# Performance work log

Measured on AMD Instinct MI355X. Metric: run time of the kernel, lower is better.

Reference implementation:

```python
import jax, jax.numpy as jnp
import numpy as np

D_MODEL = 1024
N_HEADS = 16
D_HEAD = D_MODEL // N_HEADS
D_FF = 4 * D_MODEL
EPS = 1e-5


def _layernorm(x, g, b):
    mu = jnp.mean(x, axis=-1, keepdims=True)
    var = jnp.var(x, axis=-1, keepdims=True)
    return (x - mu) * jax.lax.rsqrt(var + EPS) * g + b


def setup_inputs() -> dict:
    key = jax.random.key(0)
    ks = jax.random.split(key, 16)
    s_attn = 1.0 / np.sqrt(D_MODEL)
    s_ff1 = 1.0 / np.sqrt(D_MODEL)
    s_ff2 = 1.0 / np.sqrt(D_FF)
    inp = {
        'x': jax.random.normal(ks[0], (2, 2048, D_MODEL), dtype=jnp.float32),
        'Wq': jax.random.uniform(ks[1], (D_MODEL, D_MODEL), jnp.float32, -s_attn, s_attn),
        'bq': jax.random.uniform(ks[2], (D_MODEL,), jnp.float32, -s_attn, s_attn),
        'Wk': jax.random.uniform(ks[3], (D_MODEL, D_MODEL), jnp.float32, -s_attn, s_attn),
        'bk': jax.random.uniform(ks[4], (D_MODEL,), jnp.float32, -s_attn, s_attn),
        'Wv': jax.random.uniform(ks[5], (D_MODEL, D_MODEL), jnp.float32, -s_attn, s_attn),
        'bv': jax.random.uniform(ks[6], (D_MODEL,), jnp.float32, -s_attn, s_attn),
        'Wo': jax.random.uniform(ks[7], (D_MODEL, D_MODEL), jnp.float32, -s_attn, s_attn),
        'bo': jax.random.uniform(ks[8], (D_MODEL,), jnp.float32, -s_attn, s_attn),
        'W1': jax.random.uniform(ks[9], (D_MODEL, D_FF), jnp.float32, -s_ff1, s_ff1),
        'b1': jax.random.uniform(ks[10], (D_FF,), jnp.float32, -s_ff1, s_ff1),
        'W2': jax.random.uniform(ks[11], (D_FF, D_MODEL), jnp.float32, -s_ff2, s_ff2),
        'b2': jax.random.uniform(ks[12], (D_MODEL,), jnp.float32, -s_ff2, s_ff2),
        'ln1_g': jnp.ones((D_MODEL,), jnp.float32),
        'ln1_b': jnp.zeros((D_MODEL,), jnp.float32),
        'ln2_g': jnp.ones((D_MODEL,), jnp.float32),
        'ln2_b': jnp.zeros((D_MODEL,), jnp.float32),
    }
    return inp


def reference(x, Wq, bq, Wk, bk, Wv, bv, Wo, bo, W1, b1, W2, b2, ln1_g, ln1_b, ln2_g, ln2_b):
    B, T, D = x.shape
    scale = D_HEAD ** -0.5

    # pre-norm MHSA + residual
    h = _layernorm(x, ln1_g, ln1_b)
    def split(z):  # [B,T,D] -> [B,H,T,d_h]
        return z.reshape(B, T, N_HEADS, D_HEAD).transpose(0, 2, 1, 3)
    Q = split(h @ Wq + bq)
    K = split(h @ Wk + bk)
    V = split(h @ Wv + bv)
    scores = jnp.einsum('bhqd,bhkd->bhqk', Q, K) * scale  # [B,H,T,T]
    attn = jax.nn.softmax(scores, axis=-1)
    out = jnp.einsum('bhqk,bhkd->bhqd', attn, V)
    out = out.transpose(0, 2, 1, 3).reshape(B, T, D)
    x = x + (out @ Wo + bo)

    # pre-norm FFN + residual
    h = _layernorm(x, ln2_g, ln2_b)
    ff = jax.nn.gelu(h @ W1 + b1, approximate=False) @ W2 + b2
    return x + ff
```

## Files before the change

### kernel.cpp

```cpp
#include <hip/hip_runtime.h>
#include <math.h>

#define SEQ   2048
#define DM    1024
#define LDQKV 3072
#define MTOK  4096

typedef float  f32x4   __attribute__((ext_vector_type(4)));
typedef __bf16 bf16x8  __attribute__((ext_vector_type(8)));
typedef short  short8  __attribute__((ext_vector_type(8)));
typedef short  short4v __attribute__((ext_vector_type(4)));

__device__ __forceinline__ short f2bf(float f) {
  union { float f; unsigned u; } v; v.f = f;
  unsigned r = v.u + 0x7fffu + ((v.u >> 16) & 1u);
  return (short)(r >> 16);
}

__device__ __forceinline__ void gl_lds16(const void* g, void* l) {
  __builtin_amdgcn_global_load_lds(
      (const __attribute__((address_space(1))) void*)g,
      (__attribute__((address_space(3))) void*)l, 16, 0, 0);
}

__device__ __forceinline__ f32x4 mfma_bf16(bf16x8 a, bf16x8 b, f32x4 c) {
  return __builtin_amdgcn_mfma_f32_16x16x32_bf16(a, b, c, 0, 0, 0);
}

__global__ __launch_bounds__(256) void transpose_cast_k(
    const float* __restrict__ W, short* __restrict__ Wt, int K, int N)
{
  __shared__ float tile[32][33];
  const int n0 = blockIdx.x * 32, k0 = blockIdx.y * 32;
  const int tx = threadIdx.x & 31, ty = threadIdx.x >> 5;
#pragma unroll
  for (int i = 0; i < 4; i++)
    tile[ty + i * 8][tx] = W[(size_t)(k0 + ty + i * 8) * N + n0 + tx];
  __syncthreads();
#pragma unroll
  for (int i = 0; i < 4; i++)
    Wt[(size_t)(n0 + ty + i * 8) * K + k0 + tx] = f2bf(tile[tx][ty + i * 8]);
}

__global__ __launch_bounds__(256) void ln_k(
    const float* __restrict__ x, const float* __restrict__ g,
    const float* __restrict__ b, short* __restrict__ out)
{
  const int row = blockIdx.x;
  const int tid = threadIdx.x;
  const float4 v = ((const float4*)(x + (size_t)row * DM))[tid];
  float s  = v.x + v.y + v.z + v.w;
  float ss = v.x * v.x + v.y * v.y + v.z * v.z + v.w * v.w;
#pragma unroll
  for (int m = 32; m >= 1; m >>= 1) { s += __shfl_xor(s, m); ss += __shfl_xor(ss, m); }
  __shared__ float red[8];
  const int wid = tid >> 6;
  if ((tid & 63) == 0) { red[wid] = s; red[4 + wid] = ss; }
  __syncthreads();
  s  = red[0] + red[1] + red[2] + red[3];
  ss = red[4] + red[5] + red[6] + red[7];
  const float mu  = s * (1.f / DM);
  const float var = ss * (1.f / DM) - mu * mu;
  const float rs  = rsqrtf(var + 1e-5f);
  const float4 gv = ((const float4*)g)[tid];
  const float4 bv = ((const float4*)b)[tid];
  short4v o;
  o[0] = f2bf((v.x - mu) * rs * gv.x + bv.x);
  o[1] = f2bf((v.y - mu) * rs * gv.y + bv.y);
  o[2] = f2bf((v.z - mu) * rs * gv.z + bv.z);
  o[3] = f2bf((v.w - mu) * rs * gv.w + bv.w);
  *(short4v*)(out + (size_t)row * DM + tid * 4) = o;
}

__global__ __launch_bounds__(256) void concat_bias_k(
    const float* __restrict__ bq, const float* __restrict__ bk,
    const float* __restrict__ bv, float* __restrict__ o)
{
  int i = blockIdx.x * 256 + threadIdx.x;
  if (i < 3072) {
    float v = (i < 1024) ? bq[i] : (i < 2048 ? bk[i - 1024] : bv[i - 2048]);
    o[i] = v;
  }
}

__global__ __launch_bounds__(256) void vtrans_k(
    const short* __restrict__ V, short* __restrict__ Vt)
{
  const int b = blockIdx.z, h = blockIdx.y, t0 = blockIdx.x * 64;
  __shared__ short tile[64][72];
  const int tid = threadIdx.x;
  const int r = tid >> 2, c = (tid & 3) * 16;
  const short* src = V + (size_t)(b * SEQ + t0 + r) * LDQKV + h * 64 + c;
  *(short8*)&tile[r][c]     = *(const short8*)src;
  *(short8*)&tile[r][c + 8] = *(const short8*)(src + 8);
  __syncthreads();
  const int d = tid >> 2;
  short8 o0, o1;
#pragma unroll
  for (int k = 0; k < 8; k++) o0[k] = tile[c + k][d];
#pragma unroll
  for (int k = 0; k < 8; k++) o1[k] = tile[c + 8 + k][d];
  short* dst = Vt + (((size_t)(b * 16 + h) * 64) + d) * 2048 + t0 + c;
  *(short8*)dst       = o0;
  *(short8*)(dst + 8) = o1;
}

template <bool GELU_, bool RESID, bool OUTBF16>
__global__ __launch_bounds__(256) void gemm_bt(
    const short* __restrict__ A, const short* __restrict__ Bt,
    const float* __restrict__ bias, const float* __restrict__ resid,
    void* __restrict__ Cout, int M, int N, int K)
{
  __shared__ __align__(16) short Abuf[2][128 * 32];
  __shared__ __align__(16) short Bbuf[2][128 * 32];
  const int tid = threadIdx.x, lane = tid & 63, wid = tid >> 6;
  const int wr = wid >> 1, wc = wid & 1;
  const int bm = blockIdx.x * 128, bn = blockIdx.y * 128;

  f32x4 acc[4][4] = {};

  const int arow  = wid * 32 + (lane >> 2);
  const int acol8 = (lane & 3) * 8;
  const short* Ag0 = A  + (size_t)(bm + arow)      * K + acol8;
  const short* Ag1 = A  + (size_t)(bm + arow + 16) * K + acol8;
  const short* Bg0 = Bt + (size_t)(bn + arow)      * K + acol8;
  const short* Bg1 = Bt + (size_t)(bn + arow + 16) * K + acol8;

  const int l0 = (wid * 32) * 32, l1 = (wid * 32 + 16) * 32;

  gl_lds16(Ag0, &Abuf[0][l0]);
  gl_lds16(Ag1, &Abuf[0][l1]);
  gl_lds16(Bg0, &Bbuf[0][l0]);
  gl_lds16(Bg1, &Bbuf[0][l1]);
  __syncthreads();

  int cur = 0;
  for (int k0 = 32; k0 < K; k0 += 32) {
    const int nxt = cur ^ 1;
    gl_lds16(Ag0 + k0, &Abuf[nxt][l0]);
    gl_lds16(Ag1 + k0, &Abuf[nxt][l1]);
    gl_lds16(Bg0 + k0, &Bbuf[nxt][l0]);
    gl_lds16(Bg1 + k0, &Bbuf[nxt][l1]);

    bf16x8 a[4], b[4];
#pragma unroll
    for (int mi = 0; mi < 4; mi++)
      a[mi] = *(const bf16x8*)&Abuf[cur][(wr * 64 + mi * 16 + (lane & 15)) * 32 + (lane >> 4) * 8];
#pragma unroll
    for (int ni = 0; ni < 4; ni++)
      b[ni] = *(const bf16x8*)&Bbuf[cur][(wc * 64 + ni * 16 + (lane & 15)) * 32 + (lane >> 4) * 8];
#pragma unroll
    for (int mi = 0; mi < 4; mi++)
#pragma unroll
      for (int ni = 0; ni < 4; ni++)
        acc[mi][ni] = mfma_bf16(a[mi], b[ni], acc[mi][ni]);

    __syncthreads();
    cur = nxt;
  }

  {
    bf16x8 a[4], b[4];
#pragma unroll
    for (int mi = 0; mi < 4; mi++)
      a[mi] = *(const bf16x8*)&Abuf[cur][(wr * 64 + mi * 16 + (lane & 15)) * 32 + (lane >> 4) * 8];
#pragma unroll
    for (int ni = 0; ni < 4; ni++)
      b[ni] = *(const bf16x8*)&Bbuf[cur][(wc * 64 + ni * 16 + (lane & 15)) * 32 + (lane >> 4) * 8];
#pragma unroll
    for (int mi = 0; mi < 4; mi++)
#pragma unroll
      for (int ni = 0; ni < 4; ni++)
        acc[mi][ni] = mfma_bf16(a[mi], b[ni], acc[mi][ni]);
  }

#pragma unroll
  for (int mi = 0; mi < 4; mi++) {
#pragma unroll
    for (int ni = 0; ni < 4; ni++) {
      const int col = bn + wc * 64 + ni * 16 + (lane & 15);
      const float bs = bias[col];
#pragma unroll
      for (int j = 0; j < 4; j++) {
        const int row = bm + wr * 64 + mi * 16 + (lane >> 4) * 4 + j;
        float v = acc[mi][ni][j] + bs;
        if (GELU_) v = 0.5f * v * (1.0f + erff(v * 0.70710678118654752f));
        if (RESID) v += resid[(size_t)row * N + col];
        if (OUTBF16) ((short*)Cout)[(size_t)row * N + col] = f2bf(v);
        else         ((float*)Cout)[(size_t)row * N + col] = v;
      }
    }
  }
}

template <bool GELU_, bool RESID, bool OUTBF16>
__global__ __launch_bounds__(512) void gemm_bt8(
    const short* __restrict__ A, const short* __restrict__ Bt,
    const float* __restrict__ bias, const float* __restrict__ resid,
    void* __restrict__ Cout, int M, int N, int K)
{
  __shared__ __align__(16) short Ab[2][2][128 * 32];
  __shared__ __align__(16) short Bb[2][2][64 * 32];
  const int tid = threadIdx.x, lane = tid & 63, wid = tid >> 6;
  const int kg = wid >> 2, w2 = wid & 3;
  const int wr = w2 >> 1, wc = w2 & 1;
  const int bm = blockIdx.x * 128, bn = blockIdx.y * 64;

  f32x4 acc[4][2] = {};

  const int r_l = lane >> 2;
  const int c8  = (lane & 3) * 8;
  const short* Ag0 = A  + (size_t)(bm + w2 * 32 + r_l)      * K + c8;
  const short* Ag1 = A  + (size_t)(bm + w2 * 32 + 16 + r_l) * K + c8;
  const short* Bg0 = Bt + (size_t)(bn + w2 * 16 + r_l)      * K + c8;

  const int la0 = (w2 * 32) * 32, la1 = (w2 * 32 + 16) * 32, lb0 = (w2 * 16) * 32;
  const int kbase = kg * 32;

  gl_lds16(Ag0 + kbase, &Ab[kg][0][la0]);
  gl_lds16(Ag1 + kbase, &Ab[kg][0][la1]);
  gl_lds16(Bg0 + kbase, &Bb[kg][0][lb0]);
  __syncthreads();

  const int nsteps = K >> 6;
  int cur = 0;
  for (int i = 1; i < nsteps; ++i) {
    const int k0 = i * 64 + kbase;
    const int nxt = cur ^ 1;
    gl_lds16(Ag0 + k0, &Ab[kg][nxt][la0]);
    gl_lds16(Ag1 + k0, &Ab[kg][nxt][la1]);
    gl_lds16(Bg0 + k0, &Bb[kg][nxt][lb0]);

    bf16x8 a[4], b[2];
#pragma unroll
    for (int mi = 0; mi < 4; mi++)
      a[mi] = *(const bf16x8*)&Ab[kg][cur][(wr * 64 + mi * 16 + (lane & 15)) * 32 + (lane >> 4) * 8];
#pragma unroll
    for (int ni = 0; ni < 2; ni++)
      b[ni] = *(const bf16x8*)&Bb[kg][cur][(wc * 32 + ni * 16 + (lane & 15)) * 32 + (lane >> 4) * 8];
#pragma unroll
    for (int mi = 0; mi < 4; mi++)
#pragma unroll
      for (int ni = 0; ni < 2; ni++)
        acc[mi][ni] = mfma_bf16(a[mi], b[ni], acc[mi][ni]);

    __syncthreads();
    cur = nxt;
  }

  {
    bf16x8 a[4], b[2];
#pragma unroll
    for (int mi = 0; mi < 4; mi++)
      a[mi] = *(const bf16x8*)&Ab[kg][cur][(wr * 64 + mi * 16 + (lane & 15)) * 32 + (lane >> 4) * 8];
#pragma unroll
    for (int ni = 0; ni < 2; ni++)
      b[ni] = *(const bf16x8*)&Bb[kg][cur][(wc * 32 + ni * 16 + (lane & 15)) * 32 + (lane >> 4) * 8];
#pragma unroll
    for (int mi = 0; mi < 4; mi++)
#pragma unroll
      for (int ni = 0; ni < 2; ni++)
        acc[mi][ni] = mfma_bf16(a[mi], b[ni], acc[mi][ni]);
  }

  __syncthreads();

  float* red = (float*)&Ab[0][0][0];
  const int slot = (w2 * 64 + lane) * 8;
  if (kg == 1) {
#pragma unroll
    for (int mi = 0; mi < 4; mi++)
#pragma unroll
      for (int ni = 0; ni < 2; ni++)
        *(f32x4*)&red[(slot + mi * 2 + ni) * 4] = acc[mi][ni];
  }
  __syncthreads();
  if (kg == 0) {
#pragma unroll
    for (int mi = 0; mi < 4; mi++)
#pragma unroll
      for (int ni = 0; ni < 2; ni++)
        acc[mi][ni] += *(const f32x4*)&red[(slot + mi * 2 + ni) * 4];

#pragma unroll
    for (int mi = 0; mi < 4; mi++) {
#pragma unroll
      for (int ni = 0; ni < 2; ni++) {
        const int col = bn + wc * 32 + ni * 16 + (lane & 15);
        const float bs = bias[col];
#pragma unroll
        for (int j = 0; j < 4; j++) {
          const int row = bm + wr * 64 + mi * 16 + (lane >> 4) * 4 + j;
          float v = acc[mi][ni][j] + bs;
          if (GELU_) v = 0.5f * v * (1.0f + erff(v * 0.70710678118654752f));
          if (RESID) v += resid[(size_t)row * N + col];
          if (OUTBF16) ((short*)Cout)[(size_t)row * N + col] = f2bf(v);
          else         ((float*)Cout)[(size_t)row * N + col] = v;
        }
      }
    }
  }
}

__global__ __launch_bounds__(512, 4) void attn_k(
    const short* __restrict__ Qg, const short* __restrict__ Kg,
    const short* __restrict__ Vt, short* __restrict__ Og)
{
  const int phys = blockIdx.x;
  const int lg = (phys & 7) * 64 + (phys >> 3);
  const int q0 = (lg & 15) * 128;
  const int h  = (lg >> 4) & 15;
  const int b  = lg >> 8;

  const int tid = threadIdx.x, lane = tid & 63, w = tid >> 6;
  const int qlane = lane & 15, g = lane >> 4;

  __shared__ __align__(16) short Kl[2][128 * 64];
  __shared__ __align__(16) short Vl[2][64 * 128];

  const size_t qrow = (size_t)(b * SEQ + q0 + w * 16 + qlane) * LDQKV + h * 64;
  const bf16x8 qf0 = *(const bf16x8*)&Qg[qrow + g * 8];
  const bf16x8 qf1 = *(const bf16x8*)&Qg[qrow + 32 + g * 8];

  const int kslot = (lane & 7) ^ ((lane >> 3) & 7);
  const short* Kg_a[2];
#pragma unroll
  for (int i = 0; i < 2; i++) {
    const int r  = i * 64 + w * 8 + (lane >> 3);
    const int kc = r >> 4, gr = (r >> 2) & 3, jr = r & 3;
    const int a  = 32 * (kc & 3) + 8 * gr + 4 * (kc >> 2) + jr;
    Kg_a[i] = Kg + ((size_t)(b * SEQ) + a) * LDQKV + h * 64 + kslot * 8;
  }
  const short* Vg_s[2];
#pragma unroll
  for (int i = 0; i < 2; i++) {
    const int d  = i * 32 + w * 4 + (lane >> 4);
    const int vs = (lane & 15) ^ (d & 15);
    Vg_s[i] = Vt + ((size_t)(b * 16 + h) * 64 + d) * 2048 + vs * 8;
  }

  float m_run = -1e30f, l_run = 0.f;
  f32x4 oacc[4] = {};
  const float C = 0.125f * 1.44269504088896f;

#pragma unroll
  for (int i = 0; i < 2; i++) {
    gl_lds16(Kg_a[i], &Kl[0][(i * 64 + w * 8) * 64]);
    gl_lds16(Vg_s[i], &Vl[0][(i * 32 + w * 4) * 128]);
  }
  __syncthreads();

  int cur = 0;
  for (int kt = 0; kt < SEQ; kt += 128) {
    const int nxt = cur ^ 1;
    if (kt + 128 < SEQ) {
#pragma unroll
      for (int i = 0; i < 2; i++) {
        gl_lds16(Kg_a[i] + (size_t)(kt + 128) * LDQKV, &Kl[nxt][(i * 64 + w * 8) * 64]);
        gl_lds16(Vg_s[i] + (kt + 128),                 &Vl[nxt][(i * 32 + w * 4) * 128]);
      }
    }
    const char* KbC = (const char*)&Kl[cur][0];
    const char* VbC = (const char*)&Vl[cur][0];

    f32x4 s[8];
#pragma unroll
    for (int kc = 0; kc < 8; kc++) {
      const int kr = kc * 16 + qlane;
      const char* kp = KbC + kr * 128;
      const int sw = (kr & 7) << 4;
      bf16x8 kf0 = *(const bf16x8*)(kp + ((g * 16) ^ sw));
      bf16x8 kf1 = *(const bf16x8*)(kp + ((64 + g * 16) ^ sw));
      f32x4 z = {};
      z = mfma_bf16(kf0, qf0, z);
      z = mfma_bf16(kf1, qf1, z);
      s[kc] = z;
    }

    f32x4 m4 = s[0];
#pragma unroll
    for (int kc = 1; kc < 8; kc++) {
      m4[0] = fmaxf(m4[0], s[kc][0]); m4[1] = fmaxf(m4[1], s[kc][1]);
      m4[2] = fmaxf(m4[2], s[kc][2]); m4[3] = fmaxf(m4[3], s[kc][3]);
    }
    float mt = fmaxf(fmaxf(m4[0], m4[1]), fmaxf(m4[2], m4[3]));
    mt = fmaxf(mt, __shfl_xor(mt, 16));
    mt = fmaxf(mt, __shfl_xor(mt, 32));

    if (!__all(mt - m_run <= 40.0f)) {
      const float mnew = fmaxf(m_run, mt);
      const float r = exp2f((m_run - mnew) * C);
      m_run = mnew;
      l_run *= r;
#pragma unroll
      for (int j = 0; j < 4; j++) {
        const float rj = __shfl(r, g * 4 + j);
#pragma unroll
        for (int dt = 0; dt < 4; dt++) oacc[dt][j] *= rj;
      }
    }

    const float nmc = -m_run * C;
    float rs = 0.f;
    unsigned pw[4][4];
#pragma unroll
    for (int kc = 0; kc < 8; kc++) {
      f32x4 p;
#pragma unroll
      for (int j = 0; j < 4; j++) p[j] = exp2f(fmaf(s[kc][j], C, nmc));
      rs += (p[0] + p[1]) + (p[2] + p[3]);
      unsigned w0, w1;
      asm("v_cvt_pk_bf16_f32 %0, %1, %2" : "=v"(w0) : "v"(p[0]), "v"(p[1]));
      asm("v_cvt_pk_bf16_f32 %0, %1, %2" : "=v"(w1) : "v"(p[2]), "v"(p[3]));
      pw[kc & 3][2 * (kc >> 2) + 0] = w0;
      pw[kc & 3][2 * (kc >> 2) + 1] = w1;
    }
    rs += __shfl_xor(rs, 16);
    rs += __shfl_xor(rs, 32);
    l_run += rs;

#pragma unroll
    for (int ks = 0; ks < 4; ks++) {
      union { unsigned u[4]; bf16x8 v; } pf;
      pf.u[0] = pw[ks][0]; pf.u[1] = pw[ks][1];
      pf.u[2] = pw[ks][2]; pf.u[3] = pw[ks][3];
#pragma unroll
      for (int dt = 0; dt < 4; dt++) {
        const int vr = dt * 16 + qlane;
        bf16x8 vf = *(const bf16x8*)(VbC + vr * 256 + ((64 * ks + 16 * g) ^ ((vr & 15) << 4)));
        oacc[dt] = mfma_bf16(pf.v, vf, oacc[dt]);
      }
    }

    __syncthreads();
    cur = nxt;
  }

  const float linv = 1.f / l_run;
#pragma unroll
  for (int j = 0; j < 4; j++) {
    const float lj = __shfl(linv, g * 4 + j);
    const int tok = q0 + w * 16 + g * 4 + j;
#pragma unroll
    for (int dt = 0; dt < 4; dt++)
      Og[(size_t)(b * SEQ + tok) * DM + h * 64 + dt * 16 + qlane] = f2bf(oacc[dt][j] * lj);
  }
}

extern "C" void kernel_launch(void* const* d_in, const int* in_sizes, int n_in,
                              void* d_out, int out_size, void* d_ws, size_t ws_size,
                              hipStream_t stream)
{
  const float* x    = (const float*)d_in[0];
  const float* Wq   = (const float*)d_in[1];
  const float* bq   = (const float*)d_in[2];
  const float* Wk   = (const float*)d_in[3];
  const float* bk   = (const float*)d_in[4];
  const float* Wv   = (const float*)d_in[5];
  const float* bv   = (const float*)d_in[6];
  const float* Wo   = (const float*)d_in[7];
  const float* bo   = (const float*)d_in[8];
  const float* W1   = (const float*)d_in[9];
  const float* b1   = (const float*)d_in[10];
  const float* W2   = (const float*)d_in[11];
  const float* b2   = (const float*)d_in[12];
  const float* ln1g = (const float*)d_in[13];
  const float* ln1b = (const float*)d_in[14];
  const float* ln2g = (const float*)d_in[15];
  const float* ln2b = (const float*)d_in[16];

  char* ws = (char*)d_ws;
  const size_t MB = 1024 * 1024;
  short* Wqkvt = (short*)(ws + 0 * MB);
  short* Wqt   = Wqkvt;
  short* Wkt   = (short*)(ws + 2 * MB);
  short* Wvt   = (short*)(ws + 4 * MB);
  short* Wot   = (short*)(ws + 6 * MB);
  short* W1t   = (short*)(ws + 8 * MB);
  short* W2t   = (short*)(ws + 16 * MB);
  short* hbuf  = (short*)(ws + 24 * MB);
  short* QKV   = (short*)(ws + 32 * MB);
  short* AO    = (short*)(ws + 56 * MB);
  float* x1    = (float*)(ws + 64 * MB);
  short* Vtb   = (short*)(ws + 64 * MB);
  float* bqkv  = (float*)(ws + 80 * MB);
  short* gbuf  = (short*)(ws + 32 * MB);

  dim3 tb(256);

  transpose_cast_k<<<dim3(32, 32),  tb, 0, stream>>>(Wq, Wqt, 1024, 1024);
  transpose_cast_k<<<dim3(32, 32),  tb, 0, stream>>>(Wk, Wkt, 1024, 1024);
  transpose_cast_k<<<dim3(32, 32),  tb, 0, stream>>>(Wv, Wvt, 1024, 1024);
  transpose_cast_k<<<dim3(32, 32),  tb, 0, stream>>>(Wo, Wot, 1024, 1024);
  transpose_cast_k<<<dim3(128, 32), tb, 0, stream>>>(W1, W1t, 1024, 4096);
  transpose_cast_k<<<dim3(32, 128), tb, 0, stream>>>(W2, W2t, 4096, 1024);
  concat_bias_k<<<dim3(12), tb, 0, stream>>>(bq, bk, bv, bqkv);

  ln_k<<<dim3(MTOK), tb, 0, stream>>>(x, ln1g, ln1b, hbuf);

  gemm_bt<false, false, true><<<dim3(32, 24), tb, 0, stream>>>(
      hbuf, Wqkvt, bqkv, nullptr, QKV, MTOK, 3072, 1024);

  vtrans_k<<<dim3(32, 16, 2), tb, 0, stream>>>(QKV + 2048, Vtb);

  attn_k<<<dim3(512), dim3(512), 0, stream>>>(QKV, QKV + 1024, Vtb, AO);

  gemm_bt8<false, true, false><<<dim3(32, 16), dim3(512), 0, stream>>>(
      AO, Wot, bo, x, x1, MTOK, 1024, 1024);

  ln_k<<<dim3(MTOK), tb, 0, stream>>>(x1, ln2g, ln2b, hbuf);

  gemm_bt<true, false, true><<<dim3(32, 32), tb, 0, stream>>>(
      hbuf, W1t, b1, nullptr, gbuf, MTOK, 4096, 1024);

  gemm_bt8<false, true, false><<<dim3(32, 16), dim3(512), 0, stream>>>(
      gbuf, W2t, b2, x1, (float*)d_out, MTOK, 1024, 4096);
}
```

Before: 294.5 us.

## Add 256x256 swizzled GEMM for FFN1 and XOR-swizzle LDS in existing GEMMs

Adds a new 512-thread GEMM kernel with 256x256 output tiles, 64-wide K steps, an XOR-swizzled LDS layout, block-index remapping for L2 locality, and s_setprio around the MFMA bursts. The FFN up-projection with GELU now uses it. Separately, the existing 128-tile GEMMs get an XOR swizzle on their LDS writes and reads to cut bank conflicts. The larger tile raises data reuse per block but uses 128 KB of LDS and 128 accumulator registers per thread, which limits occupancy.

```diff
diff --git a/kernel.cpp b/kernel.cpp
--- a/kernel.cpp
+++ b/kernel.cpp
@@ -106,6 +106,103 @@
 }
 
 template <bool GELU_, bool RESID, bool OUTBF16>
+__global__ __launch_bounds__(512) void gemm256(
+    const short* __restrict__ A, const short* __restrict__ Bt,
+    const float* __restrict__ bias, const float* __restrict__ resid,
+    void* __restrict__ Cout, int M, int N, int K)
+{
+  __shared__ __align__(16) short Atile[2][256 * 64];
+  __shared__ __align__(16) short Btile[2][256 * 64];
+
+  const int tid = threadIdx.x, lane = tid & 63, wid = tid >> 6;
+  const int wm = wid >> 2, wn = wid & 3;
+
+  const int nbn = N >> 8;
+  const int chunk = gridDim.x >> 3;
+  const int swz = (blockIdx.x & 7) * chunk + (blockIdx.x >> 3);
+  const int bm = (swz / nbn) * 256;
+  const int bn = (swz % nbn) * 256;
+
+  f32x4 acc[8][4] = {};
+
+  const int srow  = wid * 8 + (lane >> 3);
+  const int sslot = (lane & 7) ^ ((lane >> 3) & 7);
+  const short* Asrc = A  + (size_t)(bm + srow) * K + sslot * 8;
+  const short* Bsrc = Bt + (size_t)(bn + srow) * K + sslot * 8;
+
+#define STAGE256(buf, k0)                                                     \
+  {                                                                           \
+    _Pragma("unroll")                                                         \
+    for (int j = 0; j < 4; j++) {                                             \
+      gl_lds16(Asrc + (size_t)(j * 64) * K + (k0), &Atile[buf][(j * 64 + wid * 8) * 64]); \
+      gl_lds16(Bsrc + (size_t)(j * 64) * K + (k0), &Btile[buf][(j * 64 + wid * 8) * 64]); \
+    }                                                                         \
+  }
+
+  const int aRowBase = (wm * 128 + (lane & 15)) * 128;
+  const int bRowBase = (wn * 64  + (lane & 15)) * 128;
+  const int slot0 = (((lane >> 4)    ) ^ (lane & 7)) * 16;
+  const int slot1 = (((lane >> 4) + 4) ^ (lane & 7)) * 16;
+
+#define COMPUTE256(buf)                                                       \
+  {                                                                           \
+    const char* Ab_ = (const char*)&Atile[buf][0];                            \
+    const char* Bb_ = (const char*)&Btile[buf][0];                            \
+    _Pragma("unroll")                                                         \
+    for (int ks = 0; ks < 2; ks++) {                                          \
+      const int sl = ks ? slot1 : slot0;                                      \
+      bf16x8 a[8], b[4];                                                      \
+      _Pragma("unroll")                                                       \
+      for (int mi = 0; mi < 8; mi++)                                          \
+        a[mi] = *(const bf16x8*)(Ab_ + aRowBase + mi * 2048 + sl);            \
+      _Pragma("unroll")                                                       \
+      for (int ni = 0; ni < 4; ni++)                                          \
+        b[ni] = *(const bf16x8*)(Bb_ + bRowBase + ni * 2048 + sl);            \
+      __builtin_amdgcn_s_setprio(1);                                          \
+      _Pragma("unroll")                                                       \
+      for (int mi = 0; mi < 8; mi++)                                          \
+        _Pragma("unroll")                                                     \
+        for (int ni = 0; ni < 4; ni++)                                        \
+          acc[mi][ni] = mfma_bf16(a[mi], b[ni], acc[mi][ni]);                 \
+      __builtin_amdgcn_s_setprio(0);                                          \
+    }                                                                         \
+  }
+
+  STAGE256(0, 0);
+  __syncthreads();
+
+  int cur = 0;
+  const int ntiles = K >> 6;
+  for (int t = 1; t < ntiles; ++t) {
+    STAGE256(cur ^ 1, t * 64);
+    COMPUTE256(cur);
+    __syncthreads();
+    cur ^= 1;
+  }
+  COMPUTE256(cur);
+
+#pragma unroll
+  for (int mi = 0; mi < 8; mi++) {
+#pragma unroll
+    for (int ni = 0; ni < 4; ni++) {
+      const int col = bn + wn * 64 + ni * 16 + (lane & 15);
+      const float bs = bias[col];
+#pragma unroll
+      for (int j = 0; j < 4; j++) {
+        const int row = bm + wm * 128 + mi * 16 + (lane >> 4) * 4 + j;
+        float v = acc[mi][ni][j] + bs;
+        if (GELU_) v = 0.5f * v * (1.0f + erff(v * 0.70710678118654752f));
+        if (RESID) v += resid[(size_t)row * N + col];
+        if (OUTBF16) ((short*)Cout)[(size_t)row * N + col] = f2bf(v);
+        else         ((float*)Cout)[(size_t)row * N + col] = v;
+      }
+    }
+  }
+#undef STAGE256
+#undef COMPUTE256
+}
+
+template <bool GELU_, bool RESID, bool OUTBF16>
 __global__ __launch_bounds__(256) void gemm_bt(
     const short* __restrict__ A, const short* __restrict__ Bt,
     const float* __restrict__ bias, const float* __restrict__ resid,
@@ -120,13 +217,14 @@
   f32x4 acc[4][4] = {};
 
   const int arow  = wid * 32 + (lane >> 2);
-  const int acol8 = (lane & 3) * 8;
+  const int acol8 = ((lane & 3) ^ ((lane >> 2) & 3)) * 8;
   const short* Ag0 = A  + (size_t)(bm + arow)      * K + acol8;
   const short* Ag1 = A  + (size_t)(bm + arow + 16) * K + acol8;
   const short* Bg0 = Bt + (size_t)(bn + arow)      * K + acol8;
   const short* Bg1 = Bt + (size_t)(bn + arow + 16) * K + acol8;
 
   const int l0 = (wid * 32) * 32, l1 = (wid * 32 + 16) * 32;
+  const int rslot = ((lane >> 4) ^ (lane & 3)) * 8;
 
   gl_lds16(Ag0, &Abuf[0][l0]);
   gl_lds16(Ag1, &Abuf[0][l1]);
@@ -145,10 +243,10 @@
     bf16x8 a[4], b[4];
 #pragma unroll
     for (int mi = 0; mi < 4; mi++)
-      a[mi] = *(const bf16x8*)&Abuf[cur][(wr * 64 + mi * 16 + (lane & 15)) * 32 + (lane >> 4) * 8];
+      a[mi] = *(const bf16x8*)&Abuf[cur][(wr * 64 + mi * 16 + (lane & 15)) * 32 + rslot];
 #pragma unroll
     for (int ni = 0; ni < 4; ni++)
-      b[ni] = *(const bf16x8*)&Bbuf[cur][(wc * 64 + ni * 16 + (lane & 15)) * 32 + (lane >> 4) * 8];
+      b[ni] = *(const bf16x8*)&Bbuf[cur][(wc * 64 + ni * 16 + (lane & 15)) * 32 + rslot];
 #pragma unroll
     for (int mi = 0; mi < 4; mi++)
 #pragma unroll
@@ -163,10 +261,10 @@
     bf16x8 a[4], b[4];
 #pragma unroll
     for (int mi = 0; mi < 4; mi++)
-      a[mi] = *(const bf16x8*)&Abuf[cur][(wr * 64 + mi * 16 + (lane & 15)) * 32 + (lane >> 4) * 8];
+      a[mi] = *(const bf16x8*)&Abuf[cur][(wr * 64 + mi * 16 + (lane & 15)) * 32 + rslot];
 #pragma unroll
     for (int ni = 0; ni < 4; ni++)
-      b[ni] = *(const bf16x8*)&Bbuf[cur][(wc * 64 + ni * 16 + (lane & 15)) * 32 + (lane >> 4) * 8];
+      b[ni] = *(const bf16x8*)&Bbuf[cur][(wc * 64 + ni * 16 + (lane & 15)) * 32 + rslot];
 #pragma unroll
     for (int mi = 0; mi < 4; mi++)
 #pragma unroll
@@ -209,13 +307,14 @@
   f32x4 acc[4][2] = {};
 
   const int r_l = lane >> 2;
-  const int c8  = (lane & 3) * 8;
+  const int c8  = ((lane & 3) ^ ((lane >> 2) & 3)) * 8;
   const short* Ag0 = A  + (size_t)(bm + w2 * 32 + r_l)      * K + c8;
   const short* Ag1 = A  + (size_t)(bm + w2 * 32 + 16 + r_l) * K + c8;
   const short* Bg0 = Bt + (size_t)(bn + w2 * 16 + r_l)      * K + c8;
 
   const int la0 = (w2 * 32) * 32, la1 = (w2 * 32 + 16) * 32, lb0 = (w2 * 16) * 32;
   const int kbase = kg * 32;
+  const int rslot = ((lane >> 4) ^ (lane & 3)) * 8;
 
   gl_lds16(Ag0 + kbase, &Ab[kg][0][la0]);
   gl_lds16(Ag1 + kbase, &Ab[kg][0][la1]);
@@ -234,10 +333,10 @@
     bf16x8 a[4], b[2];
 #pragma unroll
     for (int mi = 0; mi < 4; mi++)
-      a[mi] = *(const bf16x8*)&Ab[kg][cur][(wr * 64 + mi * 16 + (lane & 15)) * 32 + (lane >> 4) * 8];
+      a[mi] = *(const bf16x8*)&Ab[kg][cur][(wr * 64 + mi * 16 + (lane & 15)) * 32 + rslot];
 #pragma unroll
     for (int ni = 0; ni < 2; ni++)
-      b[ni] = *(const bf16x8*)&Bb[kg][cur][(wc * 32 + ni * 16 + (lane & 15)) * 32 + (lane >> 4) * 8];
+      b[ni] = *(const bf16x8*)&Bb[kg][cur][(wc * 32 + ni * 16 + (lane & 15)) * 32 + rslot];
 #pragma unroll
     for (int mi = 0; mi < 4; mi++)
 #pragma unroll
@@ -252,10 +351,10 @@
     bf16x8 a[4], b[2];
 #pragma unroll
     for (int mi = 0; mi < 4; mi++)
-      a[mi] = *(const bf16x8*)&Ab[kg][cur][(wr * 64 + mi * 16 + (lane & 15)) * 32 + (lane >> 4) * 8];
+      a[mi] = *(const bf16x8*)&Ab[kg][cur][(wr * 64 + mi * 16 + (lane & 15)) * 32 + rslot];
 #pragma unroll
     for (int ni = 0; ni < 2; ni++)
-      b[ni] = *(const bf16x8*)&Bb[kg][cur][(wc * 32 + ni * 16 + (lane & 15)) * 32 + (lane >> 4) * 8];
+      b[ni] = *(const bf16x8*)&Bb[kg][cur][(wc * 32 + ni * 16 + (lane & 15)) * 32 + rslot];
 #pragma unroll
     for (int mi = 0; mi < 4; mi++)
 #pragma unroll
@@ -510,7 +609,7 @@
 
   ln_k<<<dim3(MTOK), tb, 0, stream>>>(x1, ln2g, ln2b, hbuf);
 
-  gemm_bt<true, false, true><<<dim3(32, 32), tb, 0, stream>>>(
+  gemm256<true, false, true><<<dim3(256), dim3(512), 0, stream>>>(
       hbuf, W1t, b1, nullptr, gbuf, MTOK, 4096, 1024);
 
   gemm_bt8<false, true, false><<<dim3(32, 16), dim3(512), 0, stream>>>(
```

New measurement: 275.1 us. -6.6%, faster.
